# Kernel tuning notes

Hardware: AMD Instinct MI355X
Metric: run time of the kernel (lower is better)

## Reference

```python
import jax, jax.numpy as jnp
import numpy as np

H, D = 8, 16
HID = H * D  # hidden_channels = 128
SQRT_D = float(np.sqrt(D))


def setup_inputs() -> dict:
    key = jax.random.key(0)
    ks = iter(jax.random.split(key, 64))
    def nrm(shape, scale):
        return jax.random.normal(next(ks), shape, dtype=jnp.float32) * scale
    def rint(n, hi):
        return jax.random.randint(next(ks), (n,), 0, hi, dtype=jnp.int32)
    E = 250000
    Nh, Ni, Nt = 8000, 40000, 20000
    inp = {
        'x_herb': nrm((Nh, 400), 1.0),
        'x_ing':  nrm((Ni, 300), 1.0),
        'x_tgt':  nrm((Nt, 200), 1.0),
        # per-type input projections
        'W_herb': nrm((400, HID), 0.05), 'b_herb': jnp.zeros((HID,), jnp.float32),
        'W_ing':  nrm((300, HID), 0.06), 'b_ing':  jnp.zeros((HID,), jnp.float32),
        'W_tgt':  nrm((200, HID), 0.07), 'b_tgt':  jnp.zeros((HID,), jnp.float32),
        # HGTConv per-node-type k/q/v linears, stacked over [herb, ing, tgt]
        'Wk': nrm((3, HID, HID), 0.09), 'bk': jnp.zeros((3, HID), jnp.float32),
        'Wq': nrm((3, HID, HID), 0.09), 'bq': jnp.zeros((3, HID), jnp.float32),
        'Wv': nrm((3, HID, HID), 0.09), 'bv': jnp.zeros((3, HID), jnp.float32),
        # per-edge-type relation matrices / priors, stacked over 4 edge types
        'a_rel': nrm((4, H, D, D), 0.25),
        'm_rel': nrm((4, H, D, D), 0.25),
        'p_rel': jnp.ones((4, H), jnp.float32),
        # per-dst-node-type output linear + skip gate
        'Wa': nrm((3, HID, HID), 0.09), 'ba': jnp.zeros((3, HID), jnp.float32),
        'skip': jnp.ones((3,), jnp.float32),
        # final herb linear
        'W_out': nrm((HID, HID), 0.09), 'b_out': jnp.zeros((HID,), jnp.float32),
        # edge lists: (herb->ing contains), (ing->herb rev), (ing->tgt targets), (tgt->ing rev)
        'src_ci': rint(E, Nh), 'dst_ci': rint(E, Ni),
        'src_ic': rint(E, Ni), 'dst_ic': rint(E, Nh),
        'src_it': rint(E, Ni), 'dst_it': rint(E, Nt),
        'src_ti': rint(E, Nt), 'dst_ti': rint(E, Ni),
    }
    return inp


def _hetero_forward(x_herb, x_ing, x_tgt, W_herb, b_herb, W_ing, b_ing, W_tgt, b_tgt,
                    Wk, bk, Wq, bq, Wv, bv, a_rel, m_rel, p_rel, Wa, ba, skip,
                    W_out, b_out, src_ci, dst_ci, src_ic, dst_ic, src_it, dst_it,
                    src_ti, dst_ti):
    types = ['herb', 'ing', 'tgt']
    xs = {'herb': x_herb @ W_herb + b_herb,
          'ing':  x_ing  @ W_ing  + b_ing,
          'tgt':  x_tgt  @ W_tgt  + b_tgt}
    Ns = {t: xs[t].shape[0] for t in types}
    # per-node-type k/q/v, reshaped to [N, H, D]
    k = {t: (xs[t] @ Wk[i] + bk[i]).reshape(-1, H, D) for i, t in enumerate(types)}
    q = {t: (xs[t] @ Wq[i] + bq[i]).reshape(-1, H, D) for i, t in enumerate(types)}
    v = {t: (xs[t] @ Wv[i] + bv[i]).reshape(-1, H, D) for i, t in enumerate(types)}

    edge_defs = [  # (edge_type_id, src_type, dst_type, src_idx, dst_idx)
        (0, 'herb', 'ing', src_ci, dst_ci),
        (1, 'ing', 'herb', src_ic, dst_ic),
        (2, 'ing', 'tgt', src_it, dst_it),
        (3, 'tgt', 'ing', src_ti, dst_ti),
    ]
    contrib = {t: [] for t in types}
    for e, s, t, src, dst in edge_defs:
        # relation-specific transforms at node level, then gather per edge
        k_rel = jnp.einsum('nhd,hde->nhe', k[s], a_rel[e])  # [Ns, H, D]
        v_rel = jnp.einsum('nhd,hde->nhe', v[s], m_rel[e])  # [Ns, H, D]
        logit = (q[t][dst] * k_rel[src]).sum(-1) * (p_rel[e] / SQRT_D)  # [E, H]
        contrib[t].append((logit, v_rel[src], dst))

    out = {}
    for i, t in enumerate(types):
        logits = jnp.concatenate([c[0] for c in contrib[t]], axis=0)  # [Et, H]
        msgs = jnp.concatenate([c[1] for c in contrib[t]], axis=0)    # [Et, H, D]
        dsts = jnp.concatenate([c[2] for c in contrib[t]], axis=0)    # [Et]
        n = Ns[t]
        # segment softmax over all incoming edges of each dst node (per head)
        mx = jax.ops.segment_max(logits, dsts, num_segments=n)
        ex = jnp.exp(logits - mx[dsts])
        den = jax.ops.segment_sum(ex, dsts, num_segments=n)
        alpha = ex / (den[dsts] + 1e-16)
        agg = jax.ops.segment_sum(msgs * alpha[:, :, None], dsts, num_segments=n)
        agg = agg.reshape(n, HID)
        o = jax.nn.gelu(agg, approximate=False) @ Wa[i] + ba[i]
        g = jax.nn.sigmoid(skip[i])
        out[t] = jax.nn.relu(g * o + (1.0 - g) * xs[t])
    out_herb = out['herb'] @ W_out + b_out
    return (out_herb, out['ing'], out['tgt'])


def reference(x_herb, x_ing, x_tgt, W_herb, b_herb, W_ing, b_ing, W_tgt, b_tgt,
              Wk, bk, Wq, bq, Wv, bv, a_rel, m_rel, p_rel, Wa, ba, skip,
              W_out, b_out, src_ci, dst_ci, src_ic, dst_ic, src_it, dst_it,
              src_ti, dst_ti):
    return _hetero_forward(x_herb, x_ing, x_tgt, W_herb, b_herb, W_ing, b_ing,
                           W_tgt, b_tgt, Wk, bk, Wq, bq, Wv, bv, a_rel, m_rel,
                           p_rel, Wa, ba, skip, W_out, b_out, src_ci, dst_ci,
                           src_ic, dst_ic, src_it, dst_it, src_ti, dst_ti)
```

## Files before the change

kernel.cpp:

```cpp
#include <hip/hip_runtime.h>
#include <math.h>

#define HID 128
typedef unsigned int uint;
typedef unsigned short ushort;
typedef __attribute__((ext_vector_type(8))) short short8;
typedef __attribute__((ext_vector_type(4))) float floatx4;
typedef __attribute__((ext_vector_type(2))) float f32x2;

__device__ __forceinline__ ushort f2b(float f) {
  uint u = __float_as_uint(f);
  u += 0x7fffu + ((u >> 16) & 1u);
  return (ushort)(u >> 16);
}
__device__ __forceinline__ float b2f(ushort s) {
  return __uint_as_float(((uint)s) << 16);
}
__device__ __forceinline__ float blo(uint u) { return __uint_as_float(u << 16); }
__device__ __forceinline__ float bhi(uint u) { return __uint_as_float(u & 0xffff0000u); }
__device__ __forceinline__ f32x2 b2x2(uint u) {
  f32x2 r;
  r.x = __uint_as_float(u << 16);
  r.y = __uint_as_float(u & 0xffff0000u);
  return r;
}

__device__ __forceinline__ void gll16(const ushort* g, ushort* l) {
  __builtin_amdgcn_global_load_lds(
      (const __attribute__((address_space(1))) void*)g,
      (__attribute__((address_space(3))) void*)l, 16, 0, 0);
}

__device__ __forceinline__ size_t a_packed_us(int rr, int col) {
  int tm = rr >> 7, prow = rr & 127;
  int ptk = col >> 5, kin = col & 31;
  int sw = (kin >> 3) ^ ((prow >> 1) & 3);
  return (((size_t)tm * 4 + ptk) * 512 + (size_t)prow * 4 + sw) * 8 + (kin & 7);
}

#define CSR_CH 2048
#define CSR_SH 9

struct EdgeStreams {
  const int* src[4]; const int* dst[4];
  int off[4]; uint rel[4]; uint ldb[4];
};

struct WBlk { const float* src; ushort* dst; int K; int start; };
struct Prolog {
  int wstart, bstart, total;
  const float *Wk, *bk, *Wv, *bv, *a_rel, *m_rel, *p_rel;
  ushort* kw_dst[4];
  ushort* vw_dst[4];
  float* bcat;
  int kb_off[4], vb_off[4];
  WBlk wb[10];
  const float* bq;
  int bq_off[3];
  const int* edst[4];
  int eoff[4];
  uint* hist;
  int NBs, NBH, NBK, E;
};

__device__ void combine_rel_elem(const Prolog& P, int idx)
{
  int col  = idx & 127;
  int rest = idx >> 7;
  int row  = rest % 129;
  rest /= 129;
  int kv = rest & 1;
  int e  = rest >> 1;
  int i  = (e + 1) >> 1;
  int h = col >> 4, j = col & 15;
  const float* Wsrc = kv ? P.Wv : P.Wk;
  const float* bsrc = kv ? P.bv : P.bk;
  const float* rel  = kv ? P.m_rel : P.a_rel;
  float acc = 0.f;
  if (row < 128) {
#pragma unroll
    for (int d = 0; d < 16; ++d)
      acc += Wsrc[(size_t)i * 16384 + (size_t)row * 128 + h * 16 + d] *
             rel[((e * 8 + h) * 16 + d) * 16 + j];
  } else {
#pragma unroll
    for (int d = 0; d < 16; ++d)
      acc += bsrc[i * 128 + h * 16 + d] * rel[((e * 8 + h) * 16 + d) * 16 + j];
  }
  if (!kv) acc *= P.p_rel[e * 8 + h] * 0.36067376022224085f;
  if (row < 128) {
    ushort* dst = kv ? P.vw_dst[e] : P.kw_dst[e];
    int tk = row >> 5, chunk = (row >> 3) & 3, m = row & 7;
    int swf = chunk ^ ((col >> 1) & 3);
    dst[((tk * 512 + col * 4 + swf) << 3) + m] = f2b(acc);
  } else {
    P.bcat[(kv ? P.vb_off[e] : P.kb_off[e]) + col] = acc;
  }
}

__device__ void conv_elem(const Prolog& P, int s0)
{
  int si = 0;
#pragma unroll
  for (int k = 1; k < 10; ++k)
    if (s0 >= P.wb[k].start) si = k;
  WBlk b = P.wb[si];
  int s = s0 - b.start;
  int tk = s >> 9, o = s & 511;
  int c = o >> 2, swf = o & 3;
  int chunk = swf ^ ((c >> 1) & 3);
  int r0 = tk * 32 + chunk * 8;
  ushort tmp[8];
#pragma unroll
  for (int m = 0; m < 8; ++m) {
    int r = r0 + m;
    tmp[m] = (r < b.K) ? f2b(b.src[(size_t)r * 128 + c]) : (ushort)0;
  }
  *(short8*)&b.dst[(size_t)s * 8] = *(short8*)tmp;
}

__global__ __launch_bounds__(256)
void prologue(Prolog P)
{
  __shared__ uint h[512];
  int bI = blockIdx.x;
  if (bI < P.NBH) {
    int et = bI / P.NBs;
    int i0 = (bI - et * P.NBs) * CSR_CH;
    const int* dp = P.edst[et];
    int off = P.eoff[et];
    for (int t = threadIdx.x; t < P.NBK; t += 256) h[t] = 0;
    __syncthreads();
#pragma unroll
    for (int j = 0; j < CSR_CH / 256; ++j) {
      int idx = i0 + j * 256 + threadIdx.x;
      if (idx < P.E) atomicAdd(&h[(uint)(off + dp[idx]) >> CSR_SH], 1u);
    }
    __syncthreads();
    for (int t = threadIdx.x; t < P.NBK; t += 256)
      P.hist[(size_t)t * P.NBH + bI] = h[t];
    return;
  }
  int gtid = (bI - P.NBH) * 256 + threadIdx.x;
  if (gtid >= P.total) return;
  if (gtid >= P.bstart) {
    int j = gtid - P.bstart;
    P.bcat[P.bq_off[j >> 7] + (j & 127)] = P.bq[j];
    return;
  }
  if (gtid >= P.wstart) { conv_elem(P, gtid - P.wstart); return; }
  combine_rel_elem(P, gtid);
}

__global__ __launch_bounds__(256)
void bucket_scan(uint* __restrict__ hist, uint* __restrict__ bucketTot, int NBH)
{
  __shared__ uint ws[4];
  __shared__ uint carry_s;
  int b = blockIdx.x;
  int t = threadIdx.x, lane = t & 63, w = t >> 6;
  if (t == 0) carry_s = 0;
  __syncthreads();
  for (int base = 0; base < NBH; base += 256) {
    int i = base + t;
    uint x = (i < NBH) ? hist[(size_t)b * NBH + i] : 0u;
    uint v = x;
#pragma unroll
    for (int o = 1; o < 64; o <<= 1) {
      uint y = __shfl_up(v, o, 64);
      if (lane >= o) v += y;
    }
    if (lane == 63) ws[w] = v;
    __syncthreads();
    uint add = carry_s;
    for (int k = 0; k < w; ++k) add += ws[k];
    if (i < NBH) hist[(size_t)b * NBH + i] = add + v - x;
    __syncthreads();
    if (t == 255) carry_s = add + v;
    __syncthreads();
  }
  if (t == 0) bucketTot[b] = carry_s;
}

__device__ __forceinline__ void base_scan(const uint* __restrict__ bucketTot,
                                          uint* sb, uint* ws, int NBK)
{
  int t = threadIdx.x, lane = t & 63, w = t >> 6;
  sb[t] = (t < NBK) ? bucketTot[t] : 0u;
  sb[t + 256] = (t + 256 < NBK) ? bucketTot[t + 256] : 0u;
  __syncthreads();
  uint a0 = sb[2 * t], a1 = sb[2 * t + 1];
  uint s = a0 + a1;
  uint v = s;
#pragma unroll
  for (int o = 1; o < 64; o <<= 1) {
    uint y = __shfl_up(v, o, 64);
    if (lane >= o) v += y;
  }
  if (lane == 63) ws[w] = v;
  __syncthreads();
  uint add = 0;
  for (int k = 0; k < w; ++k) add += ws[k];
  uint e0 = add + v - s;
  sb[2 * t] = e0;
  sb[2 * t + 1] = e0 + a0;
  __syncthreads();
}

__global__ __launch_bounds__(256)
void bucket_scatter(EdgeStreams es, const uint* __restrict__ hist,
                    const uint* __restrict__ bucketTot,
                    uint2* __restrict__ inter, int NBs, int NBH, int NBK, int E)
{
  __shared__ uint sb[516];
  __shared__ uint ws[4];
  __shared__ uint cur[512];
  base_scan(bucketTot, sb, ws, NBK);
  int b = blockIdx.x;
  int et = b / NBs;
  int i0 = (b - et * NBs) * CSR_CH;
  const int* dp = es.dst[et];
  const int* sp = es.src[et];
  int off = es.off[et];
  uint rel = es.rel[et], ldb = es.ldb[et];
  for (int t = threadIdx.x; t < NBK; t += 256)
    cur[t] = sb[t] + hist[(size_t)t * NBH + b];
  __syncthreads();
#pragma unroll
  for (int j = 0; j < CSR_CH / 256; ++j) {
    int idx = i0 + j * 256 + threadIdx.x;
    if (idx < E) {
      int g = off + dp[idx];
      uint pos = atomicAdd(&cur[(uint)g >> CSR_SH], 1u);
      inter[pos] = make_uint2(rel + (uint)sp[idx] * ldb, (uint)g);
    }
  }
}

__global__ __launch_bounds__(256)
void bucket_finalize(const uint2* __restrict__ inter,
                     const uint* __restrict__ bucketTot,
                     int* __restrict__ starts, uint* __restrict__ payload,
                     int Ntot, int NBK)
{
  __shared__ uint sb[516];
  __shared__ uint ncnt[512];
  __shared__ uint ws[4];
  base_scan(bucketTot, sb, ws, NBK);
  int b = blockIdx.x;
  int g0 = b << CSR_SH;
  int t = threadIdx.x, lane = t & 63, w = t >> 6;
  uint r0 = sb[b], r1 = sb[b + 1];
  if (b == NBK - 1 && t == 0) starts[Ntot] = (int)r1;
  ncnt[t] = 0; ncnt[t + 256] = 0;
  __syncthreads();
  for (uint i = r0 + t; i < r1; i += 256)
    atomicAdd(&ncnt[inter[i].y - g0], 1u);
  __syncthreads();
  uint a0 = ncnt[2 * t], a1 = ncnt[2 * t + 1];
  uint s = a0 + a1;
  uint v = s;
#pragma unroll
  for (int o = 1; o < 64; o <<= 1) {
    uint y = __shfl_up(v, o, 64);
    if (lane >= o) v += y;
  }
  if (lane == 63) ws[w] = v;
  __syncthreads();
  uint add = r0;
  for (int k = 0; k < w; ++k) add += ws[k];
  uint e0 = add + v - s;
  int gi = g0 + 2 * t;
  if (gi < Ntot)     starts[gi]     = (int)e0;
  if (gi + 1 < Ntot) starts[gi + 1] = (int)(e0 + a0);
  ncnt[2 * t] = e0;
  ncnt[2 * t + 1] = e0 + a0;
  __syncthreads();
  for (uint i = r0 + t; i < r1; i += 256) {
    uint2 rec = inter[i];
    uint pos = atomicAdd(&ncnt[rec.y - g0], 1u);
    payload[pos] = rec.x;
  }
}

struct GemmSeg {
  const ushort* A; const ushort* B; const float* bias;
  void* out; const ushort* xsP;
  int Ktiles, ldo, Mreal, skip_idx, epi, NT, start;
  int n2; const ushort* B2; const float* bias2;
  void* out2; int ldo2, Mreal2, epi2;
  const float* Af; int Kf, Mf;
};
struct Gemm3 { GemmSeg s[3]; const float* skip; int nseg; };

__launch_bounds__(256)
__global__ void gemm_sched(Gemm3 g3)
{
  __shared__ __align__(16) ushort lds[20480];
  ushort* Xs = lds + 12288;

  int bid = blockIdx.x;
  int si = 0;
  if (g3.nseg > 1 && bid >= g3.s[1].start)
    si = (g3.nseg > 2 && bid >= g3.s[2].start) ? 2 : 1;
  const GemmSeg sg = g3.s[si];
  int local = bid - sg.start;
  int tmH = local / sg.NT, tn = local - tmH * sg.NT;
  int tm = tmH >> 1, hm = tmH & 1;

  const int t = threadIdx.x;
  const int wave = t >> 6, lane = t & 63;
  const int wn = wave * 32;
  const int l16 = lane & 15, quad = lane >> 4;
  const int Ktiles = sg.Ktiles;
  const int swz = (quad ^ ((l16 >> 1) & 3)) * 8;

  const ushort* Ahalf = sg.A + ((size_t)tm * Ktiles) * 4096 + hm * 2048;
  const ushort* Bbase = sg.B + (size_t)tn * Ktiles * 4096;

  const int aprow = t >> 2, asw = t & 3;
  const int achunk = asw ^ ((aprow >> 1) & 3);
  const int agrow = tm * 128 + hm * 64 + aprow;
  const bool arowok = (sg.Af == nullptr) || (agrow < sg.Mf);
  const float* axrow = sg.Af + (size_t)(arowok ? agrow : 0) * sg.Kf;

  floatx4 acc[4][2];
#pragma unroll
  for (int i = 0; i < 4; ++i)
#pragma unroll
    for (int j = 0; j < 2; ++j) acc[i][j] = (floatx4){0.f, 0.f, 0.f, 0.f};

  auto stageA = [&](int tk, int buf) {
    if (sg.Af == nullptr) {
      gll16(Ahalf + (size_t)tk * 4096 + wave * 512 + lane * 8,
            lds + buf * 2048 + wave * 512);
    } else {
      int gk = tk * 32 + achunk * 8;
      ushort tmp[8];
      if (arowok && gk + 8 <= sg.Kf) {
        const float* p = axrow + gk;
        float4 a = *(const float4*)p, b = *(const float4*)(p + 4);
        tmp[0] = f2b(a.x); tmp[1] = f2b(a.y); tmp[2] = f2b(a.z); tmp[3] = f2b(a.w);
        tmp[4] = f2b(b.x); tmp[5] = f2b(b.y); tmp[6] = f2b(b.z); tmp[7] = f2b(b.w);
      } else {
#pragma unroll
        for (int j = 0; j < 8; ++j) {
          int kk = gk + j;
          tmp[j] = (arowok && kk < sg.Kf) ? f2b(axrow[kk]) : (ushort)0;
        }
      }
      *(short8*)&lds[buf * 2048 + t * 8] = *(short8*)tmp;
    }
  };
  auto stageB = [&](int tk, int buf) {
#pragma unroll
    for (int j = 0; j < 2; ++j) {
      int c = wave * 2 + j;
      gll16(Bbase + (size_t)tk * 4096 + c * 512 + lane * 8,
            lds + 4096 + buf * 4096 + c * 512);
    }
  };
  auto stage2L = [&](int s2, int buf) {
#pragma unroll
    for (int j = 0; j < 2; ++j) {
      int c = wave * 2 + j;
      gll16(sg.B2 + (size_t)s2 * 4096 + c * 512 + lane * 8,
            lds + buf * 4096 + c * 512);
    }
  };

  stageB(0, 0);
  stageA(0, 0);
  __syncthreads();

  for (int tk = 0; tk < Ktiles; ++tk) {
    int buf = tk & 1;
    if (tk + 1 < Ktiles) { stageB(tk + 1, buf ^ 1); stageA(tk + 1, buf ^ 1); }

    short8 af[4], bfr[2];
#pragma unroll
    for (int i = 0; i < 4; ++i)
      af[i] = *(const short8*)&lds[buf * 2048 + (i * 16 + l16) * 32 + swz];
#pragma unroll
    for (int n = 0; n < 2; ++n)
      bfr[n] = *(const short8*)&lds[4096 + buf * 4096 + (wn + n * 16 + l16) * 32 + swz];
#pragma unroll
    for (int mi = 0; mi < 4; ++mi)
#pragma unroll
      for (int ni = 0; ni < 2; ++ni)
        acc[mi][ni] = __builtin_amdgcn_mfma_f32_16x16x32_bf16(
            bfr[ni], af[mi], acc[mi][ni], 0, 0, 0);
    __syncthreads();
  }

  if (sg.n2 > 0) stage2L(0, 0);

  const int epi = sg.epi;
  float g = 0.f, omg = 0.f;
  if (epi == 2 || epi == 3 || epi == 5) {
    float s = g3.skip[sg.skip_idx];
    g = 1.f / (1.f + __expf(-s));
    omg = 1.f - g;
  }
#pragma unroll
  for (int ni = 0; ni < 2; ++ni) {
    int cl = wn + ni * 16 + quad * 4;
    int cb = tn * 128 + cl;
    float4 b4 = *(const float4*)&sg.bias[cb];
#pragma unroll
    for (int mi = 0; mi < 4; ++mi) {
      int prow = mi * 16 + l16;
      int rr = tm * 128 + hm * 64 + prow;
      float v0 = acc[mi][ni][0] + b4.x;
      float v1 = acc[mi][ni][1] + b4.y;
      float v2 = acc[mi][ni][2] + b4.z;
      float v3 = acc[mi][ni][3] + b4.w;
      if (epi == 0) {
        uint2 o = make_uint2(((uint)f2b(v1) << 16) | f2b(v0),
                             ((uint)f2b(v3) << 16) | f2b(v2));
        *(uint2*)&((ushort*)sg.out)[(size_t)rr * sg.ldo + cb] = o;
      } else if (epi == 1) {
        if (rr < sg.Mreal)
          *(float4*)&((float*)sg.out)[(size_t)rr * sg.ldo + cb] =
              make_float4(v0, v1, v2, v3);
      } else if (epi == 2) {
        if (rr < sg.Mreal) {
          uint2 xo = *(const uint2*)&sg.xsP[a_packed_us(rr, cb)];
          float4 o;
          o.x = fmaxf(g * v0 + omg * blo(xo.x), 0.f);
          o.y = fmaxf(g * v1 + omg * bhi(xo.x), 0.f);
          o.z = fmaxf(g * v2 + omg * blo(xo.y), 0.f);
          o.w = fmaxf(g * v3 + omg * bhi(xo.y), 0.f);
          *(float4*)&((float*)sg.out)[(size_t)rr * sg.ldo + cb] = o;
        }
      } else if (epi == 3) {
        uint2 xo = *(const uint2*)&sg.xsP[a_packed_us(rr, cb)];
        uint2 o = make_uint2(
            ((uint)f2b(fmaxf(g * v1 + omg * bhi(xo.x), 0.f)) << 16) |
                   f2b(fmaxf(g * v0 + omg * blo(xo.x), 0.f)),
            ((uint)f2b(fmaxf(g * v3 + omg * bhi(xo.y), 0.f)) << 16) |
                   f2b(fmaxf(g * v2 + omg * blo(xo.y), 0.f)));
        *(uint2*)&((ushort*)sg.out)[a_packed_us(rr, cb)] = o;
      } else if (epi == 4) {
        uint2 o = make_uint2(((uint)f2b(v1) << 16) | f2b(v0),
                             ((uint)f2b(v3) << 16) | f2b(v2));
        *(uint2*)&((ushort*)sg.out)[a_packed_us(rr, cb)] = o;
        int kin = cl & 31;
        int sw2 = (kin >> 3) ^ ((prow >> 1) & 3);
        *(uint2*)&Xs[(cl >> 5) * 2048 + prow * 32 + sw2 * 8 + (kin & 7)] = o;
      } else {
        uint2 xo = *(const uint2*)&sg.xsP[a_packed_us(rr, cb)];
        uint2 o = make_uint2(
            ((uint)f2b(fmaxf(g * v1 + omg * bhi(xo.x), 0.f)) << 16) |
                   f2b(fmaxf(g * v0 + omg * blo(xo.x), 0.f)),
            ((uint)f2b(fmaxf(g * v3 + omg * bhi(xo.y), 0.f)) << 16) |
                   f2b(fmaxf(g * v2 + omg * blo(xo.y), 0.f)));
        int kin = cl & 31;
        int sw2 = (kin >> 3) ^ ((prow >> 1) & 3);
        *(uint2*)&Xs[(cl >> 5) * 2048 + prow * 32 + sw2 * 8 + (kin & 7)] = o;
      }
    }
  }

  if (sg.n2 == 0) return;
  __syncthreads();
  int total2 = sg.n2 * 4;
  floatx4 a2[4][2];
#pragma unroll
  for (int i = 0; i < 4; ++i)
#pragma unroll
    for (int j = 0; j < 2; ++j) a2[i][j] = (floatx4){0.f, 0.f, 0.f, 0.f};
  for (int s2 = 0; s2 < total2; ++s2) {
    int buf = s2 & 1;
    if (s2 + 1 < total2) stage2L(s2 + 1, buf ^ 1);
    int xb = (s2 & 3) * 2048;
    short8 af[4], bfr[2];
#pragma unroll
    for (int i = 0; i < 4; ++i)
      af[i] = *(const short8*)&Xs[xb + (i * 16 + l16) * 32 + swz];
#pragma unroll
    for (int n = 0; n < 2; ++n)
      bfr[n] = *(const short8*)&lds[buf * 4096 + (wn + n * 16 + l16) * 32 + swz];
#pragma unroll
    for (int mi = 0; mi < 4; ++mi)
#pragma unroll
      for (int ni = 0; ni < 2; ++ni)
        a2[mi][ni] = __builtin_amdgcn_mfma_f32_16x16x32_bf16(
            bfr[ni], af[mi], a2[mi][ni], 0, 0, 0);
    __syncthreads();
    if ((s2 & 3) == 3) {
      int t2 = s2 >> 2;
#pragma unroll
      for (int ni = 0; ni < 2; ++ni) {
        int cb2 = t2 * 128 + wn + ni * 16 + quad * 4;
        float4 b4 = *(const float4*)&sg.bias2[cb2];
#pragma unroll
        for (int mi = 0; mi < 4; ++mi) {
          int rr = tm * 128 + hm * 64 + mi * 16 + l16;
          float v0 = a2[mi][ni][0] + b4.x;
          float v1 = a2[mi][ni][1] + b4.y;
          float v2 = a2[mi][ni][2] + b4.z;
          float v3 = a2[mi][ni][3] + b4.w;
          if (sg.epi2 == 0) {
            uint2 o = make_uint2(((uint)f2b(v1) << 16) | f2b(v0),
                                 ((uint)f2b(v3) << 16) | f2b(v2));
            *(uint2*)&((ushort*)sg.out2)[(size_t)rr * sg.ldo2 + cb2] = o;
          } else {
            if (rr < sg.Mreal2)
              *(float4*)&((float*)sg.out2)[(size_t)rr * sg.ldo2 + cb2] =
                  make_float4(v0, v1, v2, v3);
          }
          a2[mi][ni] = (floatx4){0.f, 0.f, 0.f, 0.f};
        }
      }
    }
  }
}

struct GatherType { const ushort* q; ushort* agg; int ldq; };
struct GatherDesc { GatherType ty[3]; int n0, n1; };

__launch_bounds__(256)
__global__ void gather_all(const int* __restrict__ starts,
                           const uint* __restrict__ payload,
                           const ushort* __restrict__ kvbase,
                           GatherDesc gd, int Ntot)
{
  int wid = (blockIdx.x * 256 + threadIdx.x) >> 6;
  if (wid >= Ntot) return;
  int lane = threadIdx.x & 63;
  int g = lane >> 4, l = lane & 15;

  GatherType T;
  int d;
  if (wid < gd.n0)      { T = gd.ty[0]; d = wid; }
  else if (wid < gd.n1) { T = gd.ty[1]; d = wid - gd.n0; }
  else                  { T = gd.ty[2]; d = wid - gd.n1; }

  const char* kvb = (const char*)kvbase;
  const uint lofs = (uint)l * 16u;

  uint4 qv = *(const uint4*)(T.q + (size_t)d * T.ldq + l * 8);
  f32x2 q0 = b2x2(qv.x), q1 = b2x2(qv.y), q2 = b2x2(qv.z), q3 = b2x2(qv.w);

  int e0 = starts[wid], e1 = starts[wid + 1];
  float lsum = 0.f;
  f32x2 ac0 = {0.f, 0.f}, ac1 = {0.f, 0.f}, ac2 = {0.f, 0.f}, ac3 = {0.f, 0.f};

  for (int eb = e0; eb < e1; eb += 8) {
    int eA = eb + g, eB = eA + 4;
    bool actA = eA < e1, actB = eB < e1;
    uint pA = payload[actA ? eA : e0];
    uint pB = payload[actB ? eB : e0];
    const char* bA = kvb + (pA + lofs);
    const char* bB = kvb + (pB + lofs);
    uint4 kA = *(const uint4*)bA;
    uint4 vA = *(const uint4*)(bA + 256);
    uint4 kB = *(const uint4*)bB;
    uint4 vB = *(const uint4*)(bB + 256);

    f32x2 dA = q0 * b2x2(kA.x);
    dA = __builtin_elementwise_fma(q1, b2x2(kA.y), dA);
    dA = __builtin_elementwise_fma(q2, b2x2(kA.z), dA);
    dA = __builtin_elementwise_fma(q3, b2x2(kA.w), dA);
    f32x2 dB = q0 * b2x2(kB.x);
    dB = __builtin_elementwise_fma(q1, b2x2(kB.y), dB);
    dB = __builtin_elementwise_fma(q2, b2x2(kB.z), dB);
    dB = __builtin_elementwise_fma(q3, b2x2(kB.w), dB);
    float pa = dA.x + dA.y;
    float pb = dB.x + dB.y;
    pa += __shfl_xor(pa, 1, 64);
    pb += __shfl_xor(pb, 1, 64);
    float exA = exp2f(fminf(pa, 115.4f));
    float exB = exp2f(fminf(pb, 115.4f));
    exA = actA ? exA : 0.f;
    exB = actB ? exB : 0.f;
    lsum += exA + exB;
    f32x2 xA = {exA, exA}, xB = {exB, exB};
    ac0 = __builtin_elementwise_fma(xA, b2x2(vA.x), ac0);
    ac1 = __builtin_elementwise_fma(xA, b2x2(vA.y), ac1);
    ac2 = __builtin_elementwise_fma(xA, b2x2(vA.z), ac2);
    ac3 = __builtin_elementwise_fma(xA, b2x2(vA.w), ac3);
    ac0 = __builtin_elementwise_fma(xB, b2x2(vB.x), ac0);
    ac1 = __builtin_elementwise_fma(xB, b2x2(vB.y), ac1);
    ac2 = __builtin_elementwise_fma(xB, b2x2(vB.z), ac2);
    ac3 = __builtin_elementwise_fma(xB, b2x2(vB.w), ac3);
  }

  float s0 = ac0.x, s1 = ac0.y, s2 = ac1.x, s3 = ac1.y;
  float s4 = ac2.x, s5 = ac2.y, s6 = ac3.x, s7 = ac3.y;
#define MRG(v) v += __shfl_xor(v, 16, 64); v += __shfl_xor(v, 32, 64)
  MRG(lsum); MRG(s0); MRG(s1); MRG(s2); MRG(s3); MRG(s4); MRG(s5); MRG(s6); MRG(s7);
#undef MRG

  float inv = 1.f / (lsum + 1e-16f);
  float m0 = (g & 1) ? s2 : s0, m1 = (g & 1) ? s6 : s4;
  float n0 = (g & 1) ? s3 : s1, n1 = (g & 1) ? s7 : s5;
  float x0 = ((g & 2) ? m1 : m0) * inv;
  float x1 = ((g & 2) ? n1 : n0) * inv;
  float g0 = 0.5f * x0 * (1.f + erff(x0 * 0.70710678118654752f));
  float g1 = 0.5f * x1 * (1.f + erff(x1 * 0.70710678118654752f));
  int tm = d >> 7, row = d & 127;
  int tk = l >> 2, sw = (l & 3) ^ ((row >> 1) & 3);
  size_t us = (((size_t)tm * 4 + tk) * 512 + (size_t)row * 4 + sw) * 8 + 2 * g;
  *(uint*)(T.agg + us) = ((uint)f2b(g1) << 16) | (uint)f2b(g0);
}

extern "C" void kernel_launch(void* const* d_in, const int* in_sizes, int n_in,
                              void* d_out, int out_size, void* d_ws, size_t ws_size,
                              hipStream_t stream)
{
  const float* x_herb = (const float*)d_in[0];
  const float* x_ing  = (const float*)d_in[1];
  const float* x_tgt  = (const float*)d_in[2];
  const float* W_herb = (const float*)d_in[3];
  const float* b_herb = (const float*)d_in[4];
  const float* W_ing  = (const float*)d_in[5];
  const float* b_ing  = (const float*)d_in[6];
  const float* W_tgt  = (const float*)d_in[7];
  const float* b_tgt  = (const float*)d_in[8];
  const float* Wk     = (const float*)d_in[9];
  const float* bk     = (const float*)d_in[10];
  const float* Wq     = (const float*)d_in[11];
  const float* bq     = (const float*)d_in[12];
  const float* Wv     = (const float*)d_in[13];
  const float* bv     = (const float*)d_in[14];
  const float* a_rel  = (const float*)d_in[15];
  const float* m_rel  = (const float*)d_in[16];
  const float* p_rel  = (const float*)d_in[17];
  const float* Wa     = (const float*)d_in[18];
  const float* ba     = (const float*)d_in[19];
  const float* skip   = (const float*)d_in[20];
  const float* W_out  = (const float*)d_in[21];
  const float* b_out  = (const float*)d_in[22];
  const int* srcs[4] = {(const int*)d_in[23], (const int*)d_in[25],
                        (const int*)d_in[27], (const int*)d_in[29]};
  const int* dsts[4] = {(const int*)d_in[24], (const int*)d_in[26],
                        (const int*)d_in[28], (const int*)d_in[30]};

  const int Nh = in_sizes[0] / 400;
  const int Ni = in_sizes[1] / 300;
  const int Nt = in_sizes[2] / 200;
  const int E  = in_sizes[23];
  const int Ntot = Nh + Ni + Nt;

  const int MT_h = (Nh + 127) / 128, MT_i = (Ni + 127) / 128, MT_t = (Nt + 127) / 128;
  const int KT_h = 13, KT_i = 10, KT_t = 7;

  const int NBs = (E + CSR_CH - 1) / CSR_CH;
  const int NBH = 4 * NBs;
  const int NBK = (Ntot + (1 << CSR_SH) - 1) >> CSR_SH;

  char* base = (char*)d_ws;
  size_t off = 0;
  auto A = [&](size_t bytes) -> void* {
    void* p = base + off; off += (bytes + 255) & ~(size_t)255; return p;
  };
  ushort* xsP_h = (ushort*)A((size_t)MT_h * 4 * 8192);
  ushort* xsP_i = (ushort*)A((size_t)MT_i * 4 * 8192);
  ushort* xsP_t = (ushort*)A((size_t)MT_t * 4 * 8192);
  ushort* fused_h = (ushort*)A((size_t)MT_h * 128 * 384 * 2);
  ushort* fused_i = (ushort*)A((size_t)MT_i * 128 * 640 * 2);
  ushort* fused_t = (ushort*)A((size_t)MT_t * 128 * 384 * 2);
  ushort* aggp_h  = (ushort*)A((size_t)MT_h * 4 * 8192);
  ushort* aggp_i  = (ushort*)A((size_t)MT_i * 4 * 8192);
  ushort* aggp_t  = (ushort*)A((size_t)MT_t * 4 * 8192);
  ushort* Weff1_h = (ushort*)A((size_t)KT_h * 8192);
  ushort* Weff1_i = (ushort*)A((size_t)KT_i * 8192);
  ushort* Weff1_t = (ushort*)A((size_t)KT_t * 8192);
  ushort* Wcat_h = (ushort*)A((size_t)3 * 4 * 8192);
  ushort* Wcat_i = (ushort*)A((size_t)5 * 4 * 8192);
  ushort* Wcat_t = (ushort*)A((size_t)3 * 4 * 8192);
  float* bcat   = (float*)A(1408 * 4);
  ushort* Wa_t   = (ushort*)A((size_t)3 * 16384 * 2);
  ushort* Wout_t = (ushort*)A((size_t)16384 * 2);
  int* starts  = (int*)A((size_t)(Ntot + 4) * 4);
  uint* payload = (uint*)A((size_t)(4 * E + 8) * 4);
  uint* hist    = (uint*)A((size_t)NBK * NBH * 4);
  uint* bucketTot  = (uint*)A((size_t)NBK * 4);
  uint2* inter  = (uint2*)A((size_t)(4 * E + 8) * 8);
  (void)ws_size; (void)n_in;

  const int toff_h = 0, toff_i = Nh, toff_t = Nh + Ni;
  dim3 blk(256);

  uint fi2 = (uint)((size_t)(fused_i - fused_h) * 2);
  uint ft2 = (uint)((size_t)(fused_t - fused_h) * 2);

  Prolog P;
  P.wstart = 4 * 2 * 129 * 128;
  {
    const float* wsrc10[10] = {W_herb, W_ing, W_tgt, Wq, Wq + 16384, Wq + 32768,
                               Wa, Wa + 16384, Wa + 32768, W_out};
    ushort* wdst10[10] = {Weff1_h, Weff1_i, Weff1_t, Wcat_h, Wcat_i, Wcat_t,
                          Wa_t, Wa_t + 16384, Wa_t + 32768, Wout_t};
    int wk10[10] = {400, 300, 200, 128, 128, 128, 128, 128, 128, 128};
    int wcum = 0;
    for (int z = 0; z < 10; ++z) {
      P.wb[z] = {wsrc10[z], wdst10[z], wk10[z], wcum};
      wcum += ((wk10[z] + 31) / 32) * 512;
    }
    P.bstart = P.wstart + wcum;
  }
  P.total = P.bstart + 384;
  P.Wk = Wk; P.bk = bk; P.Wv = Wv; P.bv = bv;
  P.a_rel = a_rel; P.m_rel = m_rel; P.p_rel = p_rel;
  P.kw_dst[0] = Wcat_h + 16384; P.vw_dst[0] = Wcat_h + 32768;
  P.kw_dst[1] = Wcat_i + 16384; P.vw_dst[1] = Wcat_i + 32768;
  P.kw_dst[2] = Wcat_i + 49152; P.vw_dst[2] = Wcat_i + 65536;
  P.kw_dst[3] = Wcat_t + 16384; P.vw_dst[3] = Wcat_t + 32768;
  P.bcat = bcat;
  P.kb_off[0] = 128;  P.vb_off[0] = 256;
  P.kb_off[1] = 512;  P.vb_off[1] = 640;
  P.kb_off[2] = 768;  P.vb_off[2] = 896;
  P.kb_off[3] = 1152; P.vb_off[3] = 1280;
  P.bq = bq;
  P.bq_off[0] = 0; P.bq_off[1] = 384; P.bq_off[2] = 1024;
  P.edst[0] = dsts[0]; P.eoff[0] = toff_i;
  P.edst[1] = dsts[1]; P.eoff[1] = toff_h;
  P.edst[2] = dsts[2]; P.eoff[2] = toff_t;
  P.edst[3] = dsts[3]; P.eoff[3] = toff_i;
  P.hist = hist; P.NBs = NBs; P.NBH = NBH; P.NBK = NBK; P.E = E;
  prologue<<<NBH + (P.total + 255) / 256, blk, 0, stream>>>(P);

  EdgeStreams ES;
  ES.src[0] = srcs[0]; ES.dst[0] = dsts[0]; ES.off[0] = toff_i;
  ES.rel[0] = 256u;        ES.ldb[0] = 768u;
  ES.src[1] = srcs[1]; ES.dst[1] = dsts[1]; ES.off[1] = toff_h;
  ES.rel[1] = fi2 + 256u;  ES.ldb[1] = 1280u;
  ES.src[2] = srcs[2]; ES.dst[2] = dsts[2]; ES.off[2] = toff_t;
  ES.rel[2] = fi2 + 768u;  ES.ldb[2] = 1280u;
  ES.src[3] = srcs[3]; ES.dst[3] = dsts[3]; ES.off[3] = toff_i;
  ES.rel[3] = ft2 + 256u;  ES.ldb[3] = 768u;
  bucket_scan<<<NBK, blk, 0, stream>>>(hist, bucketTot, NBH);
  bucket_scatter<<<NBH, blk, 0, stream>>>(ES, hist, bucketTot, inter, NBs, NBH, NBK, E);
  bucket_finalize<<<NBK, blk, 0, stream>>>(inter, bucketTot, starts, payload, Ntot, NBK);

  Gemm3 G1;
  G1.skip = skip; G1.nseg = 3;
  G1.s[0] = {nullptr, Weff1_h, b_herb, xsP_h, nullptr, KT_h, 0, 0, 0, 4, 1, 0,
             3, Wcat_h, bcat + 0, fused_h, 384, 0, 0, x_herb, 400, Nh};
  G1.s[1] = {nullptr, Weff1_i, b_ing,  xsP_i, nullptr, KT_i, 0, 0, 0, 4, 1, 2 * MT_h,
             5, Wcat_i, bcat + 384, fused_i, 640, 0, 0, x_ing, 300, Ni};
  G1.s[2] = {nullptr, Weff1_t, b_tgt,  xsP_t, nullptr, KT_t, 0, 0, 0, 4, 1,
             2 * (MT_h + MT_i),
             3, Wcat_t, bcat + 1024, fused_t, 384, 0, 0, x_tgt, 200, Nt};
  gemm_sched<<<2 * (MT_h + MT_i + MT_t), blk, 0, stream>>>(G1);

  GatherDesc GD;
  GD.n0 = Nh; GD.n1 = Nh + Ni;
  GD.ty[0] = {fused_h, aggp_h, 384};
  GD.ty[1] = {fused_i, aggp_i, 640};
  GD.ty[2] = {fused_t, aggp_t, 384};
  gather_all<<<(Ntot + 3) / 4, blk, 0, stream>>>(starts, payload, fused_h, GD, Ntot);

  float* outp = (float*)d_out;
  float* out_herb = outp;
  float* out_ing  = outp + (size_t)Nh * HID;
  float* out_tgt  = outp + (size_t)(Nh + Ni) * HID;
  Gemm3 GE;
  GE.skip = skip; GE.nseg = 3;
  GE.s[0] = {aggp_h, Wa_t + 0 * 16384, ba + 0 * 128, nullptr, xsP_h,
             4, 0, 0, 0, 5, 1, 0,
             1, Wout_t, b_out, out_herb, 128, Nh, 1, nullptr, 0, 0};
  GE.s[1] = {aggp_i, Wa_t + 1 * 16384, ba + 1 * 128, out_ing, xsP_i,
             4, 128, Ni, 1, 2, 1, 2 * MT_h,
             0, nullptr, nullptr, nullptr, 0, 0, 0, nullptr, 0, 0};
  GE.s[2] = {aggp_t, Wa_t + 2 * 16384, ba + 2 * 128, out_tgt, xsP_t,
             4, 128, Nt, 2, 2, 1, 2 * (MT_h + MT_i),
             0, nullptr, nullptr, nullptr, 0, 0, 0, nullptr, 0, 0};
  gemm_sched<<<2 * (MT_h + MT_i + MT_t), blk, 0, stream>>>(GE);
  (void)out_size;
}
```

Before: 367.3 us.

## Load GEMM operand fragments directly from global memory, dropping LDS staging

The GEMM kernel stops staging A and B tiles through double-buffered LDS with global_load_lds and barriers. Each wave now reads its MFMA fragments straight from global memory, or from the fp32 input rows with inline bf16 conversion. LDS shrinks to the epilogue Xs buffer only, which removes per-tile __syncthreads and raises occupancy headroom. The cost is redundant global or L2 reads across waves and no software prefetch, so memory latency is exposed. The last K tile of the fp32 path always takes the bounds-checked scalar conversion path.

Measured after the change: 385.3 us. +4.9%, slower.

```diff
diff --git a/kernel.cpp b/kernel.cpp
--- a/kernel.cpp
+++ b/kernel.cpp
@@ -23,12 +23,6 @@
   r.x = __uint_as_float(u << 16);
   r.y = __uint_as_float(u & 0xffff0000u);
   return r;
-}
-
-__device__ __forceinline__ void gll16(const ushort* g, ushort* l) {
-  __builtin_amdgcn_global_load_lds(
-      (const __attribute__((address_space(1))) void*)g,
-      (__attribute__((address_space(3))) void*)l, 16, 0, 0);
 }
 
 __device__ __forceinline__ size_t a_packed_us(int rr, int col) {
@@ -296,8 +290,7 @@
 __launch_bounds__(256)
 __global__ void gemm_sched(Gemm3 g3)
 {
-  __shared__ __align__(16) ushort lds[20480];
-  ushort* Xs = lds + 12288;
+  __shared__ __align__(16) ushort Xs[8192];
 
   int bid = blockIdx.x;
   int si = 0;
@@ -314,15 +307,19 @@
   const int l16 = lane & 15, quad = lane >> 4;
   const int Ktiles = sg.Ktiles;
   const int swz = (quad ^ ((l16 >> 1) & 3)) * 8;
+  const int kq = quad * 8;
 
   const ushort* Ahalf = sg.A + ((size_t)tm * Ktiles) * 4096 + hm * 2048;
   const ushort* Bbase = sg.B + (size_t)tn * Ktiles * 4096;
 
-  const int aprow = t >> 2, asw = t & 3;
-  const int achunk = asw ^ ((aprow >> 1) & 3);
-  const int agrow = tm * 128 + hm * 64 + aprow;
-  const bool arowok = (sg.Af == nullptr) || (agrow < sg.Mf);
-  const float* axrow = sg.Af + (size_t)(arowok ? agrow : 0) * sg.Kf;
+  const float* xrow[4];
+  if (sg.Af != nullptr) {
+#pragma unroll
+    for (int i = 0; i < 4; ++i) {
+      int row = tm * 128 + hm * 64 + i * 16 + l16;
+      xrow[i] = sg.Af + (size_t)(row < sg.Mf ? row : 0) * sg.Kf;
+    }
+  }
 
   floatx4 acc[4][2];
 #pragma unroll
@@ -330,70 +327,48 @@
 #pragma unroll
     for (int j = 0; j < 2; ++j) acc[i][j] = (floatx4){0.f, 0.f, 0.f, 0.f};
 
-  auto stageA = [&](int tk, int buf) {
-    if (sg.Af == nullptr) {
-      gll16(Ahalf + (size_t)tk * 4096 + wave * 512 + lane * 8,
-            lds + buf * 2048 + wave * 512);
-    } else {
-      int gk = tk * 32 + achunk * 8;
-      ushort tmp[8];
-      if (arowok && gk + 8 <= sg.Kf) {
-        const float* p = axrow + gk;
-        float4 a = *(const float4*)p, b = *(const float4*)(p + 4);
-        tmp[0] = f2b(a.x); tmp[1] = f2b(a.y); tmp[2] = f2b(a.z); tmp[3] = f2b(a.w);
-        tmp[4] = f2b(b.x); tmp[5] = f2b(b.y); tmp[6] = f2b(b.z); tmp[7] = f2b(b.w);
+  const int tkLast = Ktiles - 1;
+  for (int tk = 0; tk < Ktiles; ++tk) {
+    short8 af[4], bfr[2];
+    if (sg.Af != nullptr) {
+      int gk = tk * 32 + kq;
+      if (tk < tkLast) {
+#pragma unroll
+        for (int i = 0; i < 4; ++i) {
+          float4 a = *(const float4*)(xrow[i] + gk);
+          float4 b = *(const float4*)(xrow[i] + gk + 4);
+          ushort tmp[8];
+          tmp[0] = f2b(a.x); tmp[1] = f2b(a.y); tmp[2] = f2b(a.z); tmp[3] = f2b(a.w);
+          tmp[4] = f2b(b.x); tmp[5] = f2b(b.y); tmp[6] = f2b(b.z); tmp[7] = f2b(b.w);
+          af[i] = *(short8*)tmp;
+        }
       } else {
 #pragma unroll
-        for (int j = 0; j < 8; ++j) {
-          int kk = gk + j;
-          tmp[j] = (arowok && kk < sg.Kf) ? f2b(axrow[kk]) : (ushort)0;
+        for (int i = 0; i < 4; ++i) {
+          ushort tmp[8];
+#pragma unroll
+          for (int j = 0; j < 8; ++j) {
+            int kk = gk + j;
+            tmp[j] = (kk < sg.Kf) ? f2b(xrow[i][kk]) : (ushort)0;
+          }
+          af[i] = *(short8*)tmp;
         }
       }
-      *(short8*)&lds[buf * 2048 + t * 8] = *(short8*)tmp;
+    } else {
+#pragma unroll
+      for (int i = 0; i < 4; ++i)
+        af[i] = *(const short8*)&Ahalf[(size_t)tk * 4096 + (i * 16 + l16) * 32 + swz];
     }
-  };
-  auto stageB = [&](int tk, int buf) {
-#pragma unroll
-    for (int j = 0; j < 2; ++j) {
-      int c = wave * 2 + j;
-      gll16(Bbase + (size_t)tk * 4096 + c * 512 + lane * 8,
-            lds + 4096 + buf * 4096 + c * 512);
-    }
-  };
-  auto stage2L = [&](int s2, int buf) {
-#pragma unroll
-    for (int j = 0; j < 2; ++j) {
-      int c = wave * 2 + j;
-      gll16(sg.B2 + (size_t)s2 * 4096 + c * 512 + lane * 8,
-            lds + buf * 4096 + c * 512);
-    }
-  };
-
-  stageB(0, 0);
-  stageA(0, 0);
-  __syncthreads();
-
-  for (int tk = 0; tk < Ktiles; ++tk) {
-    int buf = tk & 1;
-    if (tk + 1 < Ktiles) { stageB(tk + 1, buf ^ 1); stageA(tk + 1, buf ^ 1); }
-
-    short8 af[4], bfr[2];
-#pragma unroll
-    for (int i = 0; i < 4; ++i)
-      af[i] = *(const short8*)&lds[buf * 2048 + (i * 16 + l16) * 32 + swz];
 #pragma unroll
     for (int n = 0; n < 2; ++n)
-      bfr[n] = *(const short8*)&lds[4096 + buf * 4096 + (wn + n * 16 + l16) * 32 + swz];
+      bfr[n] = *(const short8*)&Bbase[(size_t)tk * 4096 + (wn + n * 16 + l16) * 32 + swz];
 #pragma unroll
     for (int mi = 0; mi < 4; ++mi)
 #pragma unroll
       for (int ni = 0; ni < 2; ++ni)
         acc[mi][ni] = __builtin_amdgcn_mfma_f32_16x16x32_bf16(
             bfr[ni], af[mi], acc[mi][ni], 0, 0, 0);
-    __syncthreads();
-  }
-
-  if (sg.n2 > 0) stage2L(0, 0);
+  }
 
   const int epi = sg.epi;
   float g = 0.f, omg = 0.f;
@@ -465,14 +440,11 @@
   if (sg.n2 == 0) return;
   __syncthreads();
   int total2 = sg.n2 * 4;
-  floatx4 a2[4][2];
 #pragma unroll
   for (int i = 0; i < 4; ++i)
 #pragma unroll
-    for (int j = 0; j < 2; ++j) a2[i][j] = (floatx4){0.f, 0.f, 0.f, 0.f};
+    for (int j = 0; j < 2; ++j) acc[i][j] = (floatx4){0.f, 0.f, 0.f, 0.f};
   for (int s2 = 0; s2 < total2; ++s2) {
-    int buf = s2 & 1;
-    if (s2 + 1 < total2) stage2L(s2 + 1, buf ^ 1);
     int xb = (s2 & 3) * 2048;
     short8 af[4], bfr[2];
 #pragma unroll
@@ -480,14 +452,13 @@
       af[i] = *(const short8*)&Xs[xb + (i * 16 + l16) * 32 + swz];
 #pragma unroll
     for (int n = 0; n < 2; ++n)
-      bfr[n] = *(const short8*)&lds[buf * 4096 + (wn + n * 16 + l16) * 32 + swz];
+      bfr[n] = *(const short8*)&sg.B2[(size_t)s2 * 4096 + (wn + n * 16 + l16) * 32 + swz];
 #pragma unroll
     for (int mi = 0; mi < 4; ++mi)
 #pragma unroll
       for (int ni = 0; ni < 2; ++ni)
-        a2[mi][ni] = __builtin_amdgcn_mfma_f32_16x16x32_bf16(
-            bfr[ni], af[mi], a2[mi][ni], 0, 0, 0);
-    __syncthreads();
+        acc[mi][ni] = __builtin_amdgcn_mfma_f32_16x16x32_bf16(
+            bfr[ni], af[mi], acc[mi][ni], 0, 0, 0);
     if ((s2 & 3) == 3) {
       int t2 = s2 >> 2;
 #pragma unroll
@@ -497,10 +468,10 @@
 #pragma unroll
         for (int mi = 0; mi < 4; ++mi) {
           int rr = tm * 128 + hm * 64 + mi * 16 + l16;
-          float v0 = a2[mi][ni][0] + b4.x;
-          float v1 = a2[mi][ni][1] + b4.y;
-          float v2 = a2[mi][ni][2] + b4.z;
-          float v3 = a2[mi][ni][3] + b4.w;
+          float v0 = acc[mi][ni][0] + b4.x;
+          float v1 = acc[mi][ni][1] + b4.y;
+          float v2 = acc[mi][ni][2] + b4.z;
+          float v3 = acc[mi][ni][3] + b4.w;
           if (sg.epi2 == 0) {
             uint2 o = make_uint2(((uint)f2b(v1) << 16) | f2b(v0),
                                  ((uint)f2b(v3) << 16) | f2b(v2));
@@ -510,7 +481,7 @@
               *(float4*)&((float*)sg.out2)[(size_t)rr * sg.ldo2 + cb2] =
                   make_float4(v0, v1, v2, v3);
           }
-          a2[mi][ni] = (floatx4){0.f, 0.f, 0.f, 0.f};
+          acc[mi][ni] = (floatx4){0.f, 0.f, 0.f, 0.f};
         }
       }
     }
```
